# Optimization experiments

Measured on AMD Instinct MI355X. Metric: run time of the kernel, lower is better.

## Reference

```python
import jax, jax.numpy as jnp
import numpy as np

D0, D1 = 8192, 8192          # dims of reconstructed matrix
NF = 32                      # num_feats (even)
QL = 4                       # qlevel -> 16 quantization levels


def setup_inputs() -> dict:
    key = jax.random.key(0)
    k1, k2 = jax.random.split(key, 2)
    values = jax.random.normal(k1, (1, 4, NF), dtype=jnp.float32) * (0.01 / np.sqrt(NF))
    feats = jax.random.uniform(k2, (D0 + D1, NF), dtype=jnp.float32)
    q = 1 << QL
    lo = 1.0 / (1 << (QL + 1))
    lin = jnp.linspace(lo, 1.0 - lo, q, dtype=jnp.float32)
    candidates = jnp.tile(lin.reshape(1, 1, q), (2, NF, 1))  # (order=2, NF, 16)
    scale = jnp.zeros((1,), jnp.float32)
    bias = jnp.zeros((1,), jnp.float32)
    which_axis = jnp.concatenate([
        jnp.zeros((D0,), jnp.int32),
        jnp.ones((D1,), jnp.int32),
    ])
    return {
        'values': values, 'feats': feats, 'candidates': candidates,
        'scale': scale, 'bias': bias, 'which_axis': which_axis,
        'd0': D0, 'd1': D1,
    }


def reference(values, feats, candidates, scale, bias, which_axis, d0, d1):
    nf = feats.shape[1]
    # --- prepare_inputs: scalar VQ with straight-through estimator ---
    qkeys = candidates[which_axis]                               # (N, F, Q)
    assigned = jnp.argmin(jnp.abs(feats[:, :, None] - qkeys), axis=-1)  # (N, F)
    quant = jnp.take_along_axis(qkeys, assigned[:, :, None], axis=-1)[..., 0]  # (N, F)
    # probs = -feats.detach() + (quant + feats): grad flows to feats (identity) and candidates (gather)
    probs = quant + feats - jax.lax.stop_gradient(feats)
    stacked = jnp.stack([probs, 1.0 - probs], axis=0)            # (2, N, F)
    # --- forward: batched contraction ---
    row, col = stacked[:, :d0], stacked[:, d0:]                  # (2,d0,F), (2,d1,F)
    mats = values.reshape(4, nf // 2, 2).transpose(2, 0, 1)      # (2, 4, F/2)
    # repeat_interleave(2, dim=0) -> index [0,0,1,1]
    rf = row[jnp.array([0, 0, 1, 1])].reshape(4, d0, 2, nf // 2).transpose(2, 0, 1, 3)  # (2,4,d0,F/2)
    # repeat(2,1,1,1) -> tile [c0,c1,c0,c1]
    cf = jnp.tile(col.reshape(2, d1, 2, nf // 2), (2, 1, 1, 1)).transpose(2, 0, 3, 1)   # (2,4,F/2,d1)
    ready = jnp.einsum('gaf,gaif,gafj->gij', mats, rf, cf)       # (2, d0, d1)
    return ready[0] * jnp.tanh(ready[1]) * jnp.exp(scale) + bias
```

## Files before the change

### kernel.cpp

```cpp
#include <hip/hip_runtime.h>

typedef __attribute__((ext_vector_type(8))) short bf16x8;
typedef __attribute__((ext_vector_type(4))) float f32x4;

#define NFC 32
#define DOUT 8192

#define WS_PR_SHORTS   0
#define WS_DC_SHORTS   (8192 * 32)
#define WS_VS_BYTES    (8192 * 32 * 2 + 8192 * 64 * 2)
#define WS_NEEDED      (WS_VS_BYTES + 8192 * 2 * 4)

__device__ __forceinline__ float quant16(float x) {
    float y = x * 16.0f;
    int k = (int)ceilf(y) - 1;
    k = k < 0 ? 0 : (k > 15 ? 15 : k);
    return (float)(2 * k + 1) * 0.03125f;
}
__device__ __forceinline__ short f2bf(float x) {
    unsigned int u = __float_as_uint(x);
    u = (u + 0x7fffu + ((u >> 16) & 1u)) >> 16;
    return (short)u;
}
__device__ __forceinline__ float bf2f(short h) {
    return __uint_as_float(((unsigned int)(unsigned short)h) << 16);
}

__global__ __launch_bounds__(256) void elicit_pre(
    const float* __restrict__ values,
    const float* __restrict__ feats,
    short* __restrict__ PrT,
    short* __restrict__ Dc,
    float* __restrict__ Vs)
{
    const int id = blockIdx.x * 256 + threadIdx.x;
    if (id < 8192) {
        const int r = id;
        const float* fr = &feats[(size_t)r * NFC];
        short* pb = &PrT[r * NFC];
        #pragma unroll
        for (int c = 0; c < 4; ++c) {
            float4 a = *(const float4*)&fr[c * 8];
            float4 b = *(const float4*)&fr[c * 8 + 4];
            bf16x8 q;
            q[0]=f2bf(quant16(a.x)); q[1]=f2bf(quant16(a.y)); q[2]=f2bf(quant16(a.z)); q[3]=f2bf(quant16(a.w));
            q[4]=f2bf(quant16(b.x)); q[5]=f2bf(quant16(b.y)); q[6]=f2bf(quant16(b.z)); q[7]=f2bf(quant16(b.w));
            *(bf16x8*)&pb[c * 8] = q;
        }
    } else {
        const int id2 = id - 8192;
        const int j = id2 >> 1;
        const int g = id2 & 1;
        const float* fr = &feats[(size_t)(DOUT + j) * NFC + (g << 4)];
        float x[16];
        #pragma unroll
        for (int c = 0; c < 4; ++c) {
            float4 v = *(const float4*)&fr[c * 4];
            x[c*4] = v.x; x[c*4+1] = v.y; x[c*4+2] = v.z; x[c*4+3] = v.w;
        }
        float vs = 0.0f;
        short hiA[16], loA[16];
        #pragma unroll
        for (int f = 0; f < 16; ++f) {
            float q = quant16(x[f]);
            float w0 = values[      2*f + g];
            float w1 = values[32  + 2*f + g];
            float w2 = values[64  + 2*f + g];
            float w3 = values[96  + 2*f + g];
            float d = (w0 - w2) * q + (w1 - w3) * (1.0f - q);
            vs += w2 * q + w3 * (1.0f - q);
            short h = f2bf(d);
            hiA[f] = h;
            loA[f] = f2bf(d - bf2f(h));
        }
        short* db = &Dc[j * 64 + (g << 5)];
        bf16x8 hv0, hv1, lv0, lv1;
        #pragma unroll
        for (int u = 0; u < 8; ++u) { hv0[u]=hiA[u]; hv1[u]=hiA[8+u]; lv0[u]=loA[u]; lv1[u]=loA[8+u]; }
        *(bf16x8*)&db[0]  = hv0;
        *(bf16x8*)&db[8]  = hv1;
        *(bf16x8*)&db[16] = lv0;
        *(bf16x8*)&db[24] = lv1;
        Vs[j * 2 + g] = vs;
    }
}

#define SST 68
__global__ __launch_bounds__(256, 4) void elicit_gemm(
    const short* __restrict__ PrT,
    const short* __restrict__ Dc,
    const float* __restrict__ Vs,
    const float* __restrict__ scale,
    const float* __restrict__ bias,
    float* __restrict__ out)
{
    __shared__ float Stg[4][16 * SST];

    const int t = threadIdx.x;
    const int lane = t & 63;
    const int w = t >> 6;
    const int row0 = blockIdx.y * 128 + ((w >> 1) << 6);
    const int col0 = blockIdx.x * 128 + ((w & 1) << 6);
    const int ci = lane & 15;
    const int lq = lane >> 4;

    float* S = Stg[w];

    bf16x8 Afr[4][2];
    #pragma unroll
    for (int nt = 0; nt < 4; ++nt)
        #pragma unroll
        for (int g = 0; g < 2; ++g)
            Afr[nt][g] = *(const bf16x8*)&Dc[(size_t)(col0 + nt*16 + ci) * 64 + (g << 5) + (lq << 3)];

    const float es = __expf(scale[0]);
    const float bs = bias[0];

    #pragma unroll
    for (int mt = 0; mt < 4; ++mt) {
        bf16x8 Bfr0 = *(const bf16x8*)&PrT[(size_t)(row0 + mt*16 + ci) * NFC + ((lq & 1) << 3)];
        bf16x8 Bfr1 = *(const bf16x8*)&PrT[(size_t)(row0 + mt*16 + ci) * NFC + 16 + ((lq & 1) << 3)];

        f32x4 acc[4][2] = {};
        #pragma unroll
        for (int nt = 0; nt < 4; ++nt) {
            acc[nt][0] = __builtin_amdgcn_mfma_f32_16x16x32_bf16(Afr[nt][0], Bfr0, acc[nt][0], 0, 0, 0);
            acc[nt][1] = __builtin_amdgcn_mfma_f32_16x16x32_bf16(Afr[nt][1], Bfr1, acc[nt][1], 0, 0, 0);
        }

        #pragma unroll
        for (int nt = 0; nt < 4; ++nt) {
            const int cb = col0 + nt*16 + (lq << 2);
            const f32x4 vA = *(const f32x4*)&Vs[(size_t)cb * 2];
            const f32x4 vB = *(const f32x4*)&Vs[(size_t)cb * 2 + 4];
            const float vs0[4] = {vA[0], vA[2], vB[0], vB[2]};
            const float vs1[4] = {vA[1], vA[3], vB[1], vB[3]};
            float x0[4], x1[4], th[4];
            float amax = 0.0f;
            #pragma unroll
            for (int r = 0; r < 4; ++r) {
                x0[r] = acc[nt][0][r] + vs0[r];
                x1[r] = acc[nt][1][r] + vs1[r];
                float t2 = x1[r] * x1[r];
                th[r] = x1[r] * fmaf(t2, fmaf(t2, fmaf(t2, -0.05396825f, 0.13333334f), -0.33333334f), 1.0f);
                amax = fmaxf(amax, fabsf(x1[r]));
            }
            if (__any(amax > 0.25f)) {
                #pragma unroll
                for (int r = 0; r < 4; ++r) {
                    float e2 = __expf(2.0f * x1[r]);
                    th[r] = __fdividef(e2 - 1.0f, e2 + 1.0f);
                }
            }
            f32x4 o;
            #pragma unroll
            for (int r = 0; r < 4; ++r)
                o[r] = fmaf(x0[r] * th[r], es, bs);
            *(f32x4*)&S[ci * SST + nt*16 + (lq << 2)] = o;
        }

        const int colf = ci << 2;
        #pragma unroll
        for (int it = 0; it < 4; ++it) {
            const int rl = it*4 + lq;
            f32x4 v = *(const f32x4*)&S[rl * SST + colf];
            *(f32x4*)&out[(size_t)(row0 + mt*16 + rl) * DOUT + col0 + colf] = v;
        }
    }
}

#define PR_STRIDE 56
#define DC_STRIDE 136
__global__ __launch_bounds__(256) void elicit_mfma(
    const float* __restrict__ values,
    const float* __restrict__ feats,
    const float* __restrict__ scale,
    const float* __restrict__ bias,
    float* __restrict__ out)
{
    __shared__ short Pr[128 * PR_STRIDE];
    __shared__ short Dcl[128 * DC_STRIDE];
    __shared__ float Vsl[128 * 2];
    __shared__ float Wl[128];

    const int t = threadIdx.x;
    const int row0 = blockIdx.y * 128;
    const int col0 = blockIdx.x * 128;

    if (t < 128) Wl[t] = values[t];
    {
        const int r = t >> 1;
        const int h = (t & 1) << 4;
        const float* fr = &feats[(size_t)(row0 + r) * NFC + h];
        float4 va = *(const float4*)&fr[0];
        float4 vb = *(const float4*)&fr[4];
        float4 vc = *(const float4*)&fr[8];
        float4 vd = *(const float4*)&fr[12];
        bf16x8 q0, q1;
        q0[0]=f2bf(quant16(va.x)); q0[1]=f2bf(quant16(va.y)); q0[2]=f2bf(quant16(va.z)); q0[3]=f2bf(quant16(va.w));
        q0[4]=f2bf(quant16(vb.x)); q0[5]=f2bf(quant16(vb.y)); q0[6]=f2bf(quant16(vb.z)); q0[7]=f2bf(quant16(vb.w));
        q1[0]=f2bf(quant16(vc.x)); q1[1]=f2bf(quant16(vc.y)); q1[2]=f2bf(quant16(vc.z)); q1[3]=f2bf(quant16(vc.w));
        q1[4]=f2bf(quant16(vd.x)); q1[5]=f2bf(quant16(vd.y)); q1[6]=f2bf(quant16(vd.z)); q1[7]=f2bf(quant16(vd.w));
        *(bf16x8*)&Pr[r * PR_STRIDE + h]     = q0;
        *(bf16x8*)&Pr[r * PR_STRIDE + h + 8] = q1;
    }
    __syncthreads();
    {
        const int j = t >> 1;
        const int g = t & 1;
        const float* fr = &feats[(size_t)(DOUT + col0 + j) * NFC + (g << 4)];
        short* dbase = &Dcl[j * DC_STRIDE + (g << 5)];
        float vs = 0.0f;
        #pragma unroll
        for (int c = 0; c < 4; ++c) {
            float4 xv = *(const float4*)&fr[c * 4];
            float xs[4] = {xv.x, xv.y, xv.z, xv.w};
            #pragma unroll
            for (int u = 0; u < 4; ++u) {
                const int f = c * 4 + u;
                float p = quant16(xs[u]);
                float w0 = Wl[      2*f + g];
                float w1 = Wl[32  + 2*f + g];
                float w2 = Wl[64  + 2*f + g];
                float w3 = Wl[96  + 2*f + g];
                float d = (w0 - w2) * p + (w1 - w3) * (1.0f - p);
                vs += w2 * p + w3 * (1.0f - p);
                short hi = f2bf(d);
                float lo = d - bf2f(hi);
                dbase[f]      = hi;
                dbase[16 + f] = f2bf(lo);
            }
        }
        Vsl[j * 2 + g] = vs;
    }
    __syncthreads();

    const int w  = t >> 6;
    const int lane = t & 63;
    const int wr = (w >> 1) << 6;
    const int wc = (w & 1) << 6;
    const int ci = lane & 15;
    const int lq = lane >> 4;

    bf16x8 Af[4][2];
    #pragma unroll
    for (int mt = 0; mt < 4; ++mt)
        #pragma unroll
        for (int g = 0; g < 2; ++g)
            Af[mt][g] = *(const bf16x8*)&Pr[(wr + mt*16 + ci) * PR_STRIDE + (g << 4) + ((lq & 1) << 3)];

    bf16x8 Bf[4][2];
    #pragma unroll
    for (int nt = 0; nt < 4; ++nt)
        #pragma unroll
        for (int g = 0; g < 2; ++g)
            Bf[nt][g] = *(const bf16x8*)&Dcl[(wc + nt*16 + ci) * DC_STRIDE + (g << 5) + (lq << 3)];

    f32x4 acc[4][4][2];
    #pragma unroll
    for (int nt = 0; nt < 4; ++nt) {
        float v0 = Vsl[(wc + nt*16 + ci) * 2 + 0];
        float v1 = Vsl[(wc + nt*16 + ci) * 2 + 1];
        #pragma unroll
        for (int mt = 0; mt < 4; ++mt) {
            acc[mt][nt][0] = (f32x4){v0, v0, v0, v0};
            acc[mt][nt][1] = (f32x4){v1, v1, v1, v1};
        }
    }
    #pragma unroll
    for (int mt = 0; mt < 4; ++mt)
        #pragma unroll
        for (int nt = 0; nt < 4; ++nt) {
            acc[mt][nt][0] = __builtin_amdgcn_mfma_f32_16x16x32_bf16(Af[mt][0], Bf[nt][0], acc[mt][nt][0], 0, 0, 0);
            acc[mt][nt][1] = __builtin_amdgcn_mfma_f32_16x16x32_bf16(Af[mt][1], Bf[nt][1], acc[mt][nt][1], 0, 0, 0);
        }

    const float es = __expf(scale[0]);
    const float bs = bias[0];
    #pragma unroll
    for (int mt = 0; mt < 4; ++mt) {
        const size_t rbase = (size_t)(row0 + wr + mt*16 + lq*4);
        #pragma unroll
        for (int nt = 0; nt < 4; ++nt) {
            const int gc = col0 + wc + nt*16 + ci;
            #pragma unroll
            for (int r = 0; r < 4; ++r) {
                float x1 = acc[mt][nt][1][r];
                float e2 = __expf(2.0f * x1);
                float th = __fdividef(e2 - 1.0f, e2 + 1.0f);
                out[(rbase + r) * (size_t)DOUT + gc] = acc[mt][nt][0][r] * th * es + bs;
            }
        }
    }
}

extern "C" void kernel_launch(void* const* d_in, const int* in_sizes, int n_in,
                              void* d_out, int out_size, void* d_ws, size_t ws_size,
                              hipStream_t stream) {
    const float* values = (const float*)d_in[0];
    const float* feats  = (const float*)d_in[1];
    const float* scale  = (const float*)d_in[3];
    const float* bias   = (const float*)d_in[4];
    float* out = (float*)d_out;

    if (ws_size >= (size_t)WS_NEEDED && d_ws != nullptr) {
        short* PrT = (short*)d_ws + WS_PR_SHORTS;
        short* Dcb = (short*)d_ws + WS_DC_SHORTS;
        float* Vs  = (float*)((char*)d_ws + WS_VS_BYTES);
        elicit_pre<<<dim3(96), dim3(256), 0, stream>>>(values, feats, PrT, Dcb, Vs);
        elicit_gemm<<<dim3(DOUT / 128, DOUT / 128), dim3(256), 0, stream>>>(PrT, Dcb, Vs, scale, bias, out);
    } else {
        elicit_mfma<<<dim3(DOUT / 128, DOUT / 128), dim3(256), 0, stream>>>(values, feats, scale, bias, out);
    }
}
```

Baseline: 58.37 us.

## Reshape warp tiles to 32x128 and stage Vs bias in shared memory

Each warp now covers 32 rows by the full 128 columns of the block instead of a 64x64 quadrant. Column operands (Dc fragments) are loaded once for 8 column tiles, and the per-column Vs values are loaded into shared memory once per block rather than read from global memory per tile. The staging buffer is widened so each output row is written as a 512-byte contiguous segment, giving wider coalesced stores. The trade-off is more A-fragment registers (16 bf16x8), which may pressure occupancy under launch_bounds(256,4), plus an added block-wide barrier.

```diff
diff --git a/kernel.cpp b/kernel.cpp
--- a/kernel.cpp
+++ b/kernel.cpp
@@ -85,7 +85,7 @@
     }
 }
 
-#define SST 68
+#define SSTW 132
 __global__ __launch_bounds__(256, 4) void elicit_gemm(
     const short* __restrict__ PrT,
     const short* __restrict__ Dc,
@@ -94,21 +94,25 @@
     const float* __restrict__ bias,
     float* __restrict__ out)
 {
-    __shared__ float Stg[4][16 * SST];
+    __shared__ float VsL[256];
+    __shared__ float Stg[4][16 * SSTW];
 
     const int t = threadIdx.x;
     const int lane = t & 63;
     const int w = t >> 6;
-    const int row0 = blockIdx.y * 128 + ((w >> 1) << 6);
-    const int col0 = blockIdx.x * 128 + ((w & 1) << 6);
+    const int col0 = blockIdx.x * 128;
+    const int row0 = blockIdx.y * 128 + (w << 5);
     const int ci = lane & 15;
     const int lq = lane >> 4;
 
+    VsL[t] = Vs[(size_t)col0 * 2 + t];
+    __syncthreads();
+
     float* S = Stg[w];
 
-    bf16x8 Afr[4][2];
-    #pragma unroll
-    for (int nt = 0; nt < 4; ++nt)
+    bf16x8 Afr[8][2];
+    #pragma unroll
+    for (int nt = 0; nt < 8; ++nt)
         #pragma unroll
         for (int g = 0; g < 2; ++g)
             Afr[nt][g] = *(const bf16x8*)&Dc[(size_t)(col0 + nt*16 + ci) * 64 + (g << 5) + (lq << 3)];
@@ -117,30 +121,28 @@
     const float bs = bias[0];
 
     #pragma unroll
-    for (int mt = 0; mt < 4; ++mt) {
+    for (int mt = 0; mt < 2; ++mt) {
         bf16x8 Bfr0 = *(const bf16x8*)&PrT[(size_t)(row0 + mt*16 + ci) * NFC + ((lq & 1) << 3)];
         bf16x8 Bfr1 = *(const bf16x8*)&PrT[(size_t)(row0 + mt*16 + ci) * NFC + 16 + ((lq & 1) << 3)];
 
-        f32x4 acc[4][2] = {};
-        #pragma unroll
-        for (int nt = 0; nt < 4; ++nt) {
-            acc[nt][0] = __builtin_amdgcn_mfma_f32_16x16x32_bf16(Afr[nt][0], Bfr0, acc[nt][0], 0, 0, 0);
-            acc[nt][1] = __builtin_amdgcn_mfma_f32_16x16x32_bf16(Afr[nt][1], Bfr1, acc[nt][1], 0, 0, 0);
-        }
-
-        #pragma unroll
-        for (int nt = 0; nt < 4; ++nt) {
-            const int cb = col0 + nt*16 + (lq << 2);
-            const f32x4 vA = *(const f32x4*)&Vs[(size_t)cb * 2];
-            const f32x4 vB = *(const f32x4*)&Vs[(size_t)cb * 2 + 4];
+        #pragma unroll
+        for (int nt = 0; nt < 8; ++nt) {
+            f32x4 a0 = {0.f, 0.f, 0.f, 0.f};
+            f32x4 a1 = {0.f, 0.f, 0.f, 0.f};
+            a0 = __builtin_amdgcn_mfma_f32_16x16x32_bf16(Afr[nt][0], Bfr0, a0, 0, 0, 0);
+            a1 = __builtin_amdgcn_mfma_f32_16x16x32_bf16(Afr[nt][1], Bfr1, a1, 0, 0, 0);
+
+            const int cbl = nt*16 + (lq << 2);
+            const f32x4 vA = *(const f32x4*)&VsL[cbl * 2];
+            const f32x4 vB = *(const f32x4*)&VsL[cbl * 2 + 4];
             const float vs0[4] = {vA[0], vA[2], vB[0], vB[2]};
             const float vs1[4] = {vA[1], vA[3], vB[1], vB[3]};
             float x0[4], x1[4], th[4];
             float amax = 0.0f;
             #pragma unroll
             for (int r = 0; r < 4; ++r) {
-                x0[r] = acc[nt][0][r] + vs0[r];
-                x1[r] = acc[nt][1][r] + vs1[r];
+                x0[r] = a0[r] + vs0[r];
+                x1[r] = a1[r] + vs1[r];
                 float t2 = x1[r] * x1[r];
                 th[r] = x1[r] * fmaf(t2, fmaf(t2, fmaf(t2, -0.05396825f, 0.13333334f), -0.33333334f), 1.0f);
                 amax = fmaxf(amax, fabsf(x1[r]));
@@ -156,15 +158,16 @@
             #pragma unroll
             for (int r = 0; r < 4; ++r)
                 o[r] = fmaf(x0[r] * th[r], es, bs);
-            *(f32x4*)&S[ci * SST + nt*16 + (lq << 2)] = o;
-        }
-
-        const int colf = ci << 2;
-        #pragma unroll
-        for (int it = 0; it < 4; ++it) {
-            const int rl = it*4 + lq;
-            f32x4 v = *(const f32x4*)&S[rl * SST + colf];
-            *(f32x4*)&out[(size_t)(row0 + mt*16 + rl) * DOUT + col0 + colf] = v;
+            *(f32x4*)&S[ci * SSTW + cbl] = o;
+        }
+
+        const int cf = (lane & 31) << 2;
+        const int rh = lane >> 5;
+        #pragma unroll
+        for (int it = 0; it < 8; ++it) {
+            const int rl = it*2 + rh;
+            f32x4 v = *(const f32x4*)&S[rl * SSTW + cf];
+            *(f32x4*)&out[(size_t)(row0 + mt*16 + rl) * DOUT + col0 + cf] = v;
         }
     }
 }
```

After: 58.75 us. No clear change (+0.7%).
